# Kernel optimization log

Hardware: AMD Instinct MI355X
Metric: run time of the kernel (lower is better)

## Reference

```python
import jax, jax.numpy as jnp
import numpy as np

MAX_VAL = 255.0
C1 = (0.01 * MAX_VAL) ** 2
C2 = (0.03 * MAX_VAL) ** 2


def _gauss_window(ws, sigma, channel=3):
    x = np.arange(ws, dtype=np.float64)
    g = np.exp(-((x - ws // 2) ** 2) / (2.0 * sigma ** 2))
    g = g / g.sum()
    w2 = np.outer(g, g).astype(np.float32)  # [ws, ws]
    w = np.broadcast_to(w2, (channel, 1, ws, ws)).copy()  # depthwise OIHW
    return jnp.asarray(w)


def _dwconv(x, w, pad):
    # depthwise conv2d, NCHW, groups == channels
    return jax.lax.conv_general_dilated(
        x, w, window_strides=(1, 1), padding=[(pad, pad), (pad, pad)],
        dimension_numbers=("NCHW", "OIHW", "NCHW"),
        feature_group_count=x.shape[1])


def _ssim_pair(img1, img2):
    _, c, h, w = img1.shape
    ws = min(h, w, 11)
    sigma = 1.5 * ws / 11.0
    win = _gauss_window(ws, sigma, c)
    pad = ws // 2
    mu1 = _dwconv(img1, win, pad)
    mu2 = _dwconv(img2, win, pad)
    mu1_sq, mu2_sq, mu1_mu2 = mu1 * mu1, mu2 * mu2, mu1 * mu2
    sigma1_sq = _dwconv(img1 * img1, win, pad) - mu1_sq
    sigma2_sq = _dwconv(img2 * img2, win, pad) - mu2_sq
    sigma12 = _dwconv(img1 * img2, win, pad) - mu1_mu2
    V1 = 2.0 * sigma12 + C2
    V2 = sigma1_sq + sigma2_sq + C2
    ssim_map = (2.0 * mu1_mu2 + C1) * V1 / ((mu1_sq + mu2_sq + C1) * V2)
    mcs_map = V1 / V2
    return ssim_map.mean(), mcs_map.mean()


def _avg_pool2(x):
    B, C, H, W = x.shape
    return x.reshape(B, C, H // 2, 2, W // 2, 2).mean(axis=(3, 5))


def _ms_ssim(img1, img2, levels=5):
    weight = jnp.array([0.0448, 0.2856, 0.3001, 0.2363, 0.1333], jnp.float32)
    msssim, mcs = [], []
    for _ in range(levels):
        s, m = _ssim_pair(img1, img2)
        msssim.append(s)
        mcs.append(m)
        img1 = _avg_pool2(img1)
        img2 = _avg_pool2(img2)
    msssim = jnp.stack(msssim)
    mcs = jnp.stack(mcs)
    value = jnp.prod(mcs[: levels - 1] ** weight[: levels - 1]) * msssim[levels - 1] ** weight[levels - 1]
    return 1.0 - value


def _l1_oss(img1, img2):
    _, c, h, w = img1.shape
    ws = min(h, w, 7)
    sigma = 1.1 * ws / 7.0
    win = _gauss_window(ws, sigma, c)
    return _dwconv(jnp.abs(img1 - img2), win, ws // 2).mean()


def _clr_loss(img1, img3):
    _, c, h, w = img1.shape
    ws = min(h, w, 29)
    sigma = ws / 6.0
    win = _gauss_window(ws, sigma, c)
    pad = ws // 2
    mu1 = _dwconv(img1, win, pad)
    mu3 = _dwconv(img3, win, pad)
    cw = [-0.000519, 0.07633, -0.173433, 1.435936, -1.894404, 1.556091]
    # Horner evaluation of cw[5]*x^5 + ... + cw[1]*x + cw[0]
    mu1 = ((((cw[5] * mu1 + cw[4]) * mu1 + cw[3]) * mu1 + cw[2]) * mu1 + cw[1]) * mu1 + cw[0]
    wgray = jnp.array([0.299, 0.587, 0.144], jnp.float32).reshape(1, 3, 1, 1)
    mug1 = (mu1 * wgray).sum(axis=1, keepdims=True)  # 1x1 conv over channels
    mug3 = (mu3 * wgray).sum(axis=1, keepdims=True)
    me1 = mug1.mean(axis=(2, 3), keepdims=True)
    me3 = mug3.mean(axis=(2, 3), keepdims=True)
    sc = me1 / me3
    return jnp.abs(mu1 - mu3 * sc).mean()


def setup_inputs() -> dict:
    key = jax.random.key(0)
    k1, k2, k3 = jax.random.split(key, 3)
    shape = (16, 3, 512, 512)
    return {
        "img1": jax.random.uniform(k1, shape, dtype=jnp.float32),
        "img2": jax.random.uniform(k2, shape, dtype=jnp.float32),
        "img3": jax.random.uniform(k3, shape, dtype=jnp.float32),
    }


def reference(img1, img2, img3):
    l1v = _l1_oss(img1, img2)
    clrv = _clr_loss(img1, img3)
    ssimv = _ms_ssim(img1, img2)
    return 0.4 * ssimv + 0.4 * l1v + 0.2 * clrv
```

## Files before the change

### kernel.cpp

```cpp
#include <hip/hip_runtime.h>
#include <hip/hip_fp16.h>
#include <cmath>

typedef float f2 __attribute__((ext_vector_type(2)));

struct GW7  { float g[7];  };
struct GW11 { float g[11]; };
struct GW29 { float g[29]; };

static void make_gauss(int ws, double sigma, float* out) {
    double t[32]; double s = 0.0;
    int c = ws / 2;
    for (int i = 0; i < ws; ++i) { double d = i - c; t[i] = exp(-(d * d) / (2.0 * sigma * sigma)); s += t[i]; }
    for (int i = 0; i < ws; ++i) out[i] = (float)(t[i] / s);
}

#define ACC_SLOTS 44
#define ACC_BYTES (ACC_SLOTS * 64 * sizeof(double))

__device__ __forceinline__ float poly5(float x) {
    float r = fmaf(1.556091f, x, -1.894404f);
    r = fmaf(r, x, 1.435936f);
    r = fmaf(r, x, -0.173433f);
    r = fmaf(r, x, 0.07633f);
    r = fmaf(r, x, -0.000519f);
    return r;
}

__device__ __forceinline__ float border7(int p, const GW7& gw) {
    if (p >= 3 && p <= 508) return 1.f;
    float r = 0.f;
    #pragma unroll
    for (int k = 0; k < 7; ++k) { int q = p + 3 - k; if (q >= 0 && q < 512) r += gw.g[k]; }
    return r;
}

#define SSP 49
#define SRP 33
#define CLINE 33
#define CROWS 156

template<bool SRC2, bool INTERIOR>
__device__ __forceinline__ void ssim_tile(
    const float* __restrict__ Aim, const float* __restrict__ Bim,
    const f2* __restrict__ AB, int H, int plane, int ty, int tx,
    const GW11& gw, const GW7& g7, double* __restrict__ acc, int level,
    f2* __restrict__ pooled, int Ho, f2* lds, float* red, int bid)
{
    constexpr int IN = 42;
    f2* s    = lds;
    f2* r_mu = lds;
    f2* r_sq = lds + IN * SRP;

    const int tid = threadIdx.x;
    const size_t base = (size_t)plane * H * H;
    const int oy = ty * 32 - 5, ox = tx * 32 - 5;

    {
        int y = tid / 42;
        int x = tid - y * 42;
        #pragma unroll
        for (int it = 0; it < 7; ++it) {
            if (it < 6 || tid < 228) {
                f2 v;
                if (INTERIOR) {
                    size_t o = base + (size_t)(oy + y) * H + (ox + x);
                    if (SRC2) v = AB[o];
                    else { v.x = Aim[o]; v.y = Bim[o]; }
                } else {
                    int gy = oy + y, gx = ox + x;
                    bool ok = (gy >= 0) && (gy < H) && (gx >= 0) && (gx < H);
                    size_t o = base + (size_t)gy * H + gx;
                    v = (f2){0.f, 0.f};
                    if (ok) { if (SRC2) v = AB[o]; else { v.x = Aim[o]; v.y = Bim[o]; } }
                }
                s[y * SSP + x] = v;
            }
            y += 6; x += 4; if (x >= 42) { x -= 42; ++y; }
        }
    }
    __syncthreads();

    f2 v[18];
    const int ry = tid >> 2, rx0 = (tid & 3) * 8;
    if (tid < IN * 4) {
        #pragma unroll
        for (int l = 0; l < 18; ++l) v[l] = s[ry * SSP + rx0 + l];
    }
    if (pooled) {
        int py = tid >> 4, px = tid & 15;
        int a = (5 + 2 * py) * SSP + 5 + 2 * px;
        f2 u = s[a] + s[a + 1] + s[a + SSP] + s[a + SSP + 1];
        pooled[(size_t)plane * Ho * Ho + (size_t)(ty * 16 + py) * Ho + (tx * 16 + px)] = 0.25f * u;
    }
    float l1p = 0.f;
    if (level == 0) {
        #pragma unroll
        for (int jj = 0; jj < 4; ++jj) {
            int p = jj * 256 + tid;
            int py = p >> 5, px = p & 31;
            f2 u = s[(5 + py) * SSP + 5 + px];
            float d = fabsf(u.x - u.y);
            if (INTERIOR) l1p += d;
            else l1p += border7(ty * 32 + py, g7) * border7(tx * 32 + px, g7) * d;
        }
    }
    __syncthreads();

    if (tid < IN * 4) {
        #pragma unroll
        for (int j = 0; j < 8; ++j) {
            f2 a = {0.f, 0.f};
            #pragma unroll
            for (int k = 0; k < 11; ++k) a = gw.g[k] * v[j + k] + a;
            r_mu[ry * SRP + rx0 + j] = a;
        }
        #pragma unroll
        for (int l = 0; l < 18; ++l) {
            f2 w;
            w.x = fmaf(v[l].x, v[l].x, v[l].y * v[l].y);
            w.y = v[l].x * v[l].y;
            v[l] = w;
        }
        #pragma unroll
        for (int j = 0; j < 8; ++j) {
            f2 a = {0.f, 0.f};
            #pragma unroll
            for (int k = 0; k < 11; ++k) a = gw.g[k] * v[j + k] + a;
            r_sq[ry * SRP + rx0 + j] = a;
        }
    }
    __syncthreads();

    const int y0 = (tid >> 5) * 4, x = tid & 31;
    float lss = 0.f, lmc = 0.f;
    {
        f2 mu[4], q[4];
        {
            f2 u[14];
            #pragma unroll
            for (int l = 0; l < 14; ++l) u[l] = r_mu[(y0 + l) * SRP + x];
            #pragma unroll
            for (int j = 0; j < 4; ++j) {
                f2 a = {0.f, 0.f};
                #pragma unroll
                for (int k = 0; k < 11; ++k) a = gw.g[k] * u[j + k] + a;
                mu[j] = a;
            }
        }
        {
            f2 u[14];
            #pragma unroll
            for (int l = 0; l < 14; ++l) u[l] = r_sq[(y0 + l) * SRP + x];
            #pragma unroll
            for (int j = 0; j < 4; ++j) {
                f2 a = {0.f, 0.f};
                #pragma unroll
                for (int k = 0; k < 11; ++k) a = gw.g[k] * u[j + k] + a;
                q[j] = a;
            }
        }
        #pragma unroll
        for (int j = 0; j < 4; ++j) {
            float m1 = mu[j].x, m2 = mu[j].y;
            float P = m1 * m2;
            float S = fmaf(m1, m1, m2 * m2);
            float V1 = 2.f * (q[j].y - P) + 58.5225f;
            float V2 = (q[j].x - S) + 58.5225f;
            float num = (2.f * P + 6.5025f) * V1;
            float SC = S + 6.5025f;
            float inv = __builtin_amdgcn_rcpf(SC * V2);
            lss = fmaf(num, inv, lss);
            lmc = fmaf(V1 * SC, inv, lmc);
        }
    }
    #pragma unroll
    for (int o = 32; o > 0; o >>= 1) {
        lss += __shfl_down(lss, o); lmc += __shfl_down(lmc, o); l1p += __shfl_down(l1p, o);
    }
    if ((tid & 63) == 0) {
        int g = tid >> 6;
        red[g * 3] = lss; red[g * 3 + 1] = lmc; red[g * 3 + 2] = l1p;
    }
    __syncthreads();
    if (tid == 0) {
        float a = red[0] + red[3] + red[6] + red[9];
        float m = red[1] + red[4] + red[7] + red[10];
        int stripe = bid & 63;
        atomicAdd(&acc[(0 + level) * 64 + stripe], (double)a);
        atomicAdd(&acc[(5 + level) * 64 + stripe], (double)m);
        if (level == 0) {
            float l1 = red[2] + red[5] + red[8] + red[11];
            atomicAdd(&acc[10 * 64 + stripe], (double)l1);
        }
    }
}

template<bool SRC2>
__global__ __launch_bounds__(256, 8) void ssim_kernel(
    const float* __restrict__ Aim, const float* __restrict__ Bim, const f2* __restrict__ AB,
    int H, int tpp, int tilesX, GW11 gw, GW7 g7, double* __restrict__ acc, int level,
    f2* __restrict__ pooled, int Ho)
{
    __shared__ f2 lds[2 * 42 * SRP];
    __shared__ float red[12];
    const int bid = blockIdx.x;
    const int plane = bid / tpp;
    const int t = bid - plane * tpp;
    const int ty = t / tilesX, tx = t - ty * tilesX;
    const bool interior = (ty > 0) && (ty < tilesX - 1) && (tx > 0) && (tx < tilesX - 1);
    if (interior)
        ssim_tile<SRC2, true >(Aim, Bim, AB, H, plane, ty, tx, gw, g7, acc, level, pooled, Ho, lds, red, bid);
    else
        ssim_tile<SRC2, false>(Aim, Bim, AB, H, plane, ty, tx, gw, g7, acc, level, pooled, Ho, lds, red, bid);
}

template<bool CCLEAN>
__device__ __forceinline__ void clr_strip(
    const float* __restrict__ img1, const float* __restrict__ img3,
    int plane, int tx, int q, const GW29& gw, __half2* buf, float* red,
    double* __restrict__ acc, __half2* __restrict__ pbuf, int bid)
{
    const int tid = threadIdx.x;
    const int base_row = q * 128;
    const int b = plane / 3, c = plane - b * 3;
    const float wg = (c == 0) ? 0.299f : (c == 1 ? 0.587f : 0.144f);
    const size_t base = (size_t)plane * (512 * 512);
    const int rrow = tid >> 2, xq = tid & 3;
    const int c0 = tx * 8 + xq * 2 - 4;

    auto rowconv = [&](int rel) {
        __half2* dst = buf + (rel + 14) * CLINE + xq * 8;
        const int lr = base_row + rel;
        if (lr < 0 || lr >= 512) {
            #pragma unroll
            for (int j = 0; j < 8; ++j) dst[j] = __floats2half2_rn(0.f, 0.f);
            return;
        }
        const float4* row1 = (const float4*)(img1 + base + (size_t)lr * 512);
        const float4* row3 = (const float4*)(img3 + base + (size_t)lr * 512);
        float w[40];
        float o1[8];
        #pragma unroll
        for (int k = 0; k < 10; ++k) {
            float4 f;
            if (CCLEAN) f = row1[c0 + k];
            else {
                int cc = c0 + k;
                f = (float4){0.f, 0.f, 0.f, 0.f};
                if (cc >= 0 && cc < 128) f = row1[cc];
            }
            w[4 * k] = f.x; w[4 * k + 1] = f.y; w[4 * k + 2] = f.z; w[4 * k + 3] = f.w;
        }
        #pragma unroll
        for (int j = 0; j < 8; ++j) {
            float a = 0.f;
            #pragma unroll
            for (int k = 0; k < 29; ++k) a = fmaf(gw.g[k], w[2 + j + k], a);
            o1[j] = a;
        }
        #pragma unroll
        for (int k = 0; k < 10; ++k) {
            float4 f;
            if (CCLEAN) f = row3[c0 + k];
            else {
                int cc = c0 + k;
                f = (float4){0.f, 0.f, 0.f, 0.f};
                if (cc >= 0 && cc < 128) f = row3[cc];
            }
            w[4 * k] = f.x; w[4 * k + 1] = f.y; w[4 * k + 2] = f.z; w[4 * k + 3] = f.w;
        }
        #pragma unroll
        for (int j = 0; j < 8; ++j) {
            float a = 0.f;
            #pragma unroll
            for (int k = 0; k < 29; ++k) a = fmaf(gw.g[k], w[2 + j + k], a);
            dst[j] = __floats2half2_rn(o1[j], a);
        }
    };

    rowconv(-14 + rrow);
    __syncthreads();

    float p1 = 0.f, p3 = 0.f;
    const int x = tid & 31;
    #pragma unroll
    for (int ck = 0; ck < 2; ++ck) {
        int rel = 50 + 64 * ck + rrow;
        if (rel <= 141) rowconv(rel);
        __syncthreads();
        #pragma unroll
        for (int g = 0; g < 2; ++g) {
            const int y0 = 64 * ck + g * 32 + (tid >> 5) * 4;
            f2 u[32];
            #pragma unroll
            for (int l = 0; l < 32; ++l) {
                float2 tf = __half22float2(buf[(y0 + l) * CLINE + x]);
                u[l] = (f2){tf.x, tf.y};
            }
            #pragma unroll
            for (int j = 0; j < 4; ++j) {
                f2 a = {0.f, 0.f};
                #pragma unroll
                for (int k = 0; k < 29; ++k) a = gw.g[k] * u[j + k] + a;
                float p = poly5(a.x);
                p1 += p; p3 += a.y;
                pbuf[base + (size_t)(base_row + y0 + j) * 512 + (tx * 32 + x)] =
                    __floats2half2_rn(p, a.y);
            }
        }
    }

    p1 *= wg; p3 *= wg;
    #pragma unroll
    for (int o = 32; o > 0; o >>= 1) { p1 += __shfl_down(p1, o); p3 += __shfl_down(p3, o); }
    if ((tid & 63) == 0) { red[(tid >> 6) * 2] = p1; red[(tid >> 6) * 2 + 1] = p3; }
    __syncthreads();
    if (tid == 0) {
        float a1 = red[0] + red[2] + red[4] + red[6];
        float a3 = red[1] + red[3] + red[5] + red[7];
        int stripe = bid & 63;
        atomicAdd(&acc[(12 + b) * 64 + stripe], (double)a1);
        atomicAdd(&acc[(28 + b) * 64 + stripe], (double)a3);
    }
}

__global__ __launch_bounds__(256, 8) void fused_l0(
    const float* __restrict__ img1, const float* __restrict__ img2,
    const float* __restrict__ img3,
    GW11 g11, GW7 g7, GW29 g29,
    __half2* __restrict__ pbuf, f2* __restrict__ pooled, double* __restrict__ acc)
{
    __shared__ f2 lds[2 * 42 * SRP];
    __shared__ float red[12];
    const int bid = blockIdx.x;
    const int q5 = bid / 5;

    if (bid - q5 * 5 == 0) {
        const int cid = q5;
        __half2* buf = (__half2*)lds;
        const int plane = cid >> 6, rr = cid & 63;
        const int tx = rr >> 2, q = rr & 3;
        if (tx >= 1 && tx <= 14)
            clr_strip<true >(img1, img3, plane, tx, q, g29, buf, red, acc, pbuf, bid);
        else
            clr_strip<false>(img1, img3, plane, tx, q, g29, buf, red, acc, pbuf, bid);
        return;
    }

    const int sid = bid - q5 - 1;
    const int plane = sid >> 8;
    const int t = sid & 255;
    const int ty = t >> 4, tx = t & 15;
    const bool interior = (ty >= 1) && (ty <= 14) && (tx >= 1) && (tx <= 14);
    if (interior)
        ssim_tile<false, true >(img1, img2, nullptr, 512, plane, ty, tx, g11, g7, acc, 0, pooled, 256, lds, red, bid);
    else
        ssim_tile<false, false>(img1, img2, nullptr, 512, plane, ty, tx, g11, g7, acc, 0, pooled, 256, lds, red, bid);
}

#define CRP 33
#define RING 128
template<int MODE>
__global__ __launch_bounds__(256) void clr_conv(
    const float* __restrict__ img1, const float* __restrict__ img3,
    __half2* __restrict__ pbuf, GW29 gw, double* __restrict__ acc)
{
    __shared__ f2 r[RING * CRP];
    __shared__ float red[8];
    __shared__ float sc_sh;

    const int tid = threadIdx.x, bid = blockIdx.x;
    const int plane = bid >> 4, tx = bid & 15;
    const int b = plane / 3, c = plane - b * 3;
    const float wg = (c == 0) ? 0.299f : (c == 1 ? 0.587f : 0.144f);
    const size_t base = (size_t)plane * (512 * 512);

    if (MODE == 2 && tid < 64) {
        double m1 = acc[(12 + b) * 64 + tid];
        double m3 = acc[(28 + b) * 64 + tid];
        #pragma unroll
        for (int o = 32; o > 0; o >>= 1) { m1 += __shfl_down(m1, o); m3 += __shfl_down(m3, o); }
        if (tid == 0) sc_sh = (float)(m1 / m3);
    }

    const int rrow = tid >> 2, xq = tid & 3;
    const int c0 = tx * 8 + xq * 2 - 4;

    auto rowconv = [&](int lr) {
        const int ri = ((lr + RING) & (RING - 1)) * CRP + xq * 8;
        if (lr < 0 || lr >= 512) {
            #pragma unroll
            for (int j = 0; j < 8; ++j) r[ri + j] = (f2){0.f, 0.f};
            return;
        }
        const float4* row1 = (const float4*)(img1 + base + (size_t)lr * 512);
        const float4* row3 = (const float4*)(img3 + base + (size_t)lr * 512);
        float w[40];
        float o1[8];
        #pragma unroll
        for (int k = 0; k < 10; ++k) {
            int cc = c0 + k;
            float4 f = {0.f, 0.f, 0.f, 0.f};
            if (cc >= 0 && cc < 128) f = row1[cc];
            w[4 * k] = f.x; w[4 * k + 1] = f.y; w[4 * k + 2] = f.z; w[4 * k + 3] = f.w;
        }
        #pragma unroll
        for (int j = 0; j < 8; ++j) {
            float a = 0.f;
            #pragma unroll
            for (int k = 0; k < 29; ++k) a = fmaf(gw.g[k], w[2 + j + k], a);
            o1[j] = a;
        }
        #pragma unroll
        for (int k = 0; k < 10; ++k) {
            int cc = c0 + k;
            float4 f = {0.f, 0.f, 0.f, 0.f};
            if (cc >= 0 && cc < 128) f = row3[cc];
            w[4 * k] = f.x; w[4 * k + 1] = f.y; w[4 * k + 2] = f.z; w[4 * k + 3] = f.w;
        }
        #pragma unroll
        for (int j = 0; j < 8; ++j) {
            float a = 0.f;
            #pragma unroll
            for (int k = 0; k < 29; ++k) a = fmaf(gw.g[k], w[2 + j + k], a);
            r[ri + j] = (f2){o1[j], a};
        }
    };

    rowconv(-14 + rrow);
    __syncthreads();

    float p1 = 0.f, p3 = 0.f;
    const int x = tid & 31;
    #pragma unroll 1
    for (int ck = 0; ck < 8; ++ck) {
        {
            int lr = 50 + 64 * ck + rrow;
            if (lr <= 525) rowconv(lr);
        }
        __syncthreads();
        #pragma unroll
        for (int g = 0; g < 2; ++g) {
            const int y0 = 64 * ck + g * 32 + (tid >> 5) * 4;
            f2 u[32];
            #pragma unroll
            for (int l = 0; l < 32; ++l)
                u[l] = r[(((y0 - 14 + l) + RING) & (RING - 1)) * CRP + x];
            #pragma unroll
            for (int j = 0; j < 4; ++j) {
                f2 a = {0.f, 0.f};
                #pragma unroll
                for (int k = 0; k < 29; ++k) a = gw.g[k] * u[j + k] + a;
                float p = poly5(a.x);
                if (MODE == 2) {
                    p1 += fabsf(p - a.y * sc_sh);
                } else {
                    p1 += p; p3 += a.y;
                }
            }
        }
        if (ck < 7) __syncthreads();
    }

    if (MODE != 2) { p1 *= wg; p3 *= wg; }
    #pragma unroll
    for (int o = 32; o > 0; o >>= 1) { p1 += __shfl_down(p1, o); p3 += __shfl_down(p3, o); }
    if ((tid & 63) == 0) { red[(tid >> 6) * 2] = p1; red[(tid >> 6) * 2 + 1] = p3; }
    __syncthreads();
    if (tid == 0) {
        float a1 = red[0] + red[2] + red[4] + red[6];
        int stripe = bid & 63;
        if (MODE == 2) {
            atomicAdd(&acc[11 * 64 + stripe], (double)a1);
        } else {
            float a3 = red[1] + red[3] + red[5] + red[7];
            atomicAdd(&acc[(12 + b) * 64 + stripe], (double)a1);
            atomicAdd(&acc[(28 + b) * 64 + stripe], (double)a3);
        }
    }
}

__global__ __launch_bounds__(256) void clr_fin(
    const __half2* __restrict__ pbuf, double* __restrict__ acc)
{
    __shared__ float red[4];
    __shared__ float sc_sh;
    const int tid = threadIdx.x, bid = blockIdx.x;
    const int b = bid / 192, sub = bid - b * 192;
    if (tid < 64) {
        double m1 = acc[(12 + b) * 64 + tid];
        double m3 = acc[(28 + b) * 64 + tid];
        #pragma unroll
        for (int o = 32; o > 0; o >>= 1) { m1 += __shfl_down(m1, o); m3 += __shfl_down(m3, o); }
        if (tid == 0) sc_sh = (float)(m1 / m3);
    }
    __syncthreads();
    const float sc = sc_sh;
    const size_t bo = (size_t)b * 786432 + (size_t)sub * 4096;
    float s = 0.f;
    #pragma unroll
    for (int it = 0; it < 8; ++it) {
        size_t i = bo + it * 512 + tid * 2;
        float2 a = __half22float2(pbuf[i]);
        float2 c = __half22float2(pbuf[i + 1]);
        s += fabsf(a.x - a.y * sc) + fabsf(c.x - c.y * sc);
    }
    #pragma unroll
    for (int o = 32; o > 0; o >>= 1) s += __shfl_down(s, o);
    if ((tid & 63) == 0) red[tid >> 6] = s;
    __syncthreads();
    if (tid == 0)
        atomicAdd(&acc[11 * 64 + (bid & 63)], (double)(red[0] + red[1] + red[2] + red[3]));
}

__global__ void finalize_kernel(const double* __restrict__ acc, float* __restrict__ out)
{
    __shared__ double sums[ACC_SLOTS];
    int t = threadIdx.x;
    if (t < ACC_SLOTS) {
        double s = 0.0;
        for (int i = 0; i < 64; ++i) s += acc[t * 64 + i];
        sums[t] = s;
    }
    __syncthreads();
    if (t == 0) {
        const double w[5] = {0.0448, 0.2856, 0.3001, 0.2363, 0.1333};
        double value = 1.0;
        for (int l = 0; l < 5; ++l) {
            double dim = (double)(512 >> l);
            double cnt = 48.0 * dim * dim;
            double mval = (l < 4) ? (sums[5 + l] / cnt) : (sums[l] / cnt);
            value *= pow(mval, w[l]);
        }
        double n0 = 48.0 * 512.0 * 512.0;
        double l1v = sums[10] / n0;
        double clrv = sums[11] / n0;
        out[0] = (float)(0.4 * (1.0 - value) + 0.4 * l1v + 0.2 * clrv);
    }
}

extern "C" void kernel_launch(void* const* d_in, const int* in_sizes, int n_in,
                              void* d_out, int out_size, void* d_ws, size_t ws_size,
                              hipStream_t stream)
{
    (void)in_sizes; (void)n_in; (void)out_size;
    const float* img1 = (const float*)d_in[0];
    const float* img2 = (const float*)d_in[1];
    const float* img3 = (const float*)d_in[2];
    float* out = (float*)d_out;
    double* acc = (double*)d_ws;

    GW11 g11; make_gauss(11, 1.5, g11.g);
    GW7  g7;  make_gauss(7, 1.1, g7.g);
    GW29 g29; make_gauss(29, 29.0 / 6.0, g29.g);

    hipMemsetAsync(d_ws, 0, ACC_BYTES, stream);

    f2* pyr = (f2*)((char*)d_ws + 32768);
    size_t offs[4];
    offs[0] = 0;
    offs[1] = offs[0] + (size_t)48 * 256 * 256;
    offs[2] = offs[1] + (size_t)48 * 128 * 128;
    offs[3] = offs[2] + (size_t)48 * 64 * 64;
    const size_t PYRF2 = offs[3] + (size_t)48 * 32 * 32;

    const size_t poff = 32768 + PYRF2 * sizeof(f2);
    const size_t PBYTES = (size_t)48 * 512 * 512 * sizeof(__half2);
    __half2* pbuf = (__half2*)((char*)d_ws + poff);
    const bool bigws = (ws_size >= poff + PBYTES);

    if (bigws) {
        fused_l0<<<15360, 256, 0, stream>>>(img1, img2, img3, g11, g7, g29,
                                            pbuf, pyr + offs[0], acc);
    } else {
        ssim_kernel<false><<<12288, 256, 0, stream>>>(
            img1, img2, nullptr, 512, 256, 16, g11, g7, acc, 0, pyr + offs[0], 256);
        clr_conv<1><<<768, 256, 0, stream>>>(img1, img3, pbuf, g29, acc);
    }

    const f2* cur = pyr + offs[0];
    int H = 256;
    for (int l = 1; l < 5; ++l) {
        int tilesX = H / 32; int tpp = tilesX * tilesX;
        f2* pooled = (l < 4) ? (pyr + offs[l]) : nullptr;
        int Ho = H / 2;
        ssim_kernel<true><<<48 * tpp, 256, 0, stream>>>(
            nullptr, nullptr, cur, H, tpp, tilesX, g11, g7, acc, l, pooled, Ho);
        cur = pooled; H = Ho;
    }

    if (bigws) {
        clr_fin<<<3072, 256, 0, stream>>>(pbuf, acc);
    } else {
        clr_conv<2><<<768, 256, 0, stream>>>(img1, img3, pbuf, g29, acc);
    }

    finalize_kernel<<<1, 64, 0, stream>>>(acc, out);
}
```

Measured before the change: 217.4 us.

## Drop interior/border template specializations, streaming vertical conv, relax launch bounds

```diff
diff --git a/kernel.cpp b/kernel.cpp
--- a/kernel.cpp
+++ b/kernel.cpp
@@ -40,7 +40,7 @@
 #define CLINE 33
 #define CROWS 156
 
-template<bool SRC2, bool INTERIOR>
+template<bool SRC2>
 __device__ __forceinline__ void ssim_tile(
     const float* __restrict__ Aim, const float* __restrict__ Bim,
     const f2* __restrict__ AB, int H, int plane, int ty, int tx,
@@ -56,28 +56,17 @@
     const size_t base = (size_t)plane * H * H;
     const int oy = ty * 32 - 5, ox = tx * 32 - 5;
 
-    {
-        int y = tid / 42;
-        int x = tid - y * 42;
-        #pragma unroll
-        for (int it = 0; it < 7; ++it) {
-            if (it < 6 || tid < 228) {
-                f2 v;
-                if (INTERIOR) {
-                    size_t o = base + (size_t)(oy + y) * H + (ox + x);
-                    if (SRC2) v = AB[o];
-                    else { v.x = Aim[o]; v.y = Bim[o]; }
-                } else {
-                    int gy = oy + y, gx = ox + x;
-                    bool ok = (gy >= 0) && (gy < H) && (gx >= 0) && (gx < H);
-                    size_t o = base + (size_t)gy * H + gx;
-                    v = (f2){0.f, 0.f};
-                    if (ok) { if (SRC2) v = AB[o]; else { v.x = Aim[o]; v.y = Bim[o]; } }
-                }
-                s[y * SSP + x] = v;
-            }
-            y += 6; x += 4; if (x >= 42) { x -= 42; ++y; }
-        }
+    for (int i = tid; i < IN * IN; i += 256) {
+        int y = i / IN, x = i - y * IN;
+        int gy = oy + y, gx = ox + x;
+        bool ok = (gy >= 0) && (gy < H) && (gx >= 0) && (gx < H);
+        size_t o = base + (size_t)gy * H + gx;
+        f2 v = {0.f, 0.f};
+        if (ok) {
+            if (SRC2) v = AB[o];
+            else { v.x = Aim[o]; v.y = Bim[o]; }
+        }
+        s[y * SSP + x] = v;
     }
     __syncthreads();
 
@@ -100,9 +89,7 @@
             int p = jj * 256 + tid;
             int py = p >> 5, px = p & 31;
             f2 u = s[(5 + py) * SSP + 5 + px];
-            float d = fabsf(u.x - u.y);
-            if (INTERIOR) l1p += d;
-            else l1p += border7(ty * 32 + py, g7) * border7(tx * 32 + px, g7) * d;
+            l1p += border7(ty * 32 + py, g7) * border7(tx * 32 + px, g7) * fabsf(u.x - u.y);
         }
     }
     __syncthreads();
@@ -197,7 +184,7 @@
 }
 
 template<bool SRC2>
-__global__ __launch_bounds__(256, 8) void ssim_kernel(
+__global__ __launch_bounds__(256) void ssim_kernel(
     const float* __restrict__ Aim, const float* __restrict__ Bim, const f2* __restrict__ AB,
     int H, int tpp, int tilesX, GW11 gw, GW7 g7, double* __restrict__ acc, int level,
     f2* __restrict__ pooled, int Ho)
@@ -208,14 +195,9 @@
     const int plane = bid / tpp;
     const int t = bid - plane * tpp;
     const int ty = t / tilesX, tx = t - ty * tilesX;
-    const bool interior = (ty > 0) && (ty < tilesX - 1) && (tx > 0) && (tx < tilesX - 1);
-    if (interior)
-        ssim_tile<SRC2, true >(Aim, Bim, AB, H, plane, ty, tx, gw, g7, acc, level, pooled, Ho, lds, red, bid);
-    else
-        ssim_tile<SRC2, false>(Aim, Bim, AB, H, plane, ty, tx, gw, g7, acc, level, pooled, Ho, lds, red, bid);
-}
-
-template<bool CCLEAN>
+    ssim_tile<SRC2>(Aim, Bim, AB, H, plane, ty, tx, gw, g7, acc, level, pooled, Ho, lds, red, bid);
+}
+
 __device__ __forceinline__ void clr_strip(
     const float* __restrict__ img1, const float* __restrict__ img3,
     int plane, int tx, int q, const GW29& gw, __half2* buf, float* red,
@@ -243,13 +225,9 @@
         float o1[8];
         #pragma unroll
         for (int k = 0; k < 10; ++k) {
-            float4 f;
-            if (CCLEAN) f = row1[c0 + k];
-            else {
-                int cc = c0 + k;
-                f = (float4){0.f, 0.f, 0.f, 0.f};
-                if (cc >= 0 && cc < 128) f = row1[cc];
-            }
+            int cc = c0 + k;
+            float4 f = {0.f, 0.f, 0.f, 0.f};
+            if (cc >= 0 && cc < 128) f = row1[cc];
             w[4 * k] = f.x; w[4 * k + 1] = f.y; w[4 * k + 2] = f.z; w[4 * k + 3] = f.w;
         }
         #pragma unroll
@@ -261,13 +239,9 @@
         }
         #pragma unroll
         for (int k = 0; k < 10; ++k) {
-            float4 f;
-            if (CCLEAN) f = row3[c0 + k];
-            else {
-                int cc = c0 + k;
-                f = (float4){0.f, 0.f, 0.f, 0.f};
-                if (cc >= 0 && cc < 128) f = row3[cc];
-            }
+            int cc = c0 + k;
+            float4 f = {0.f, 0.f, 0.f, 0.f};
+            if (cc >= 0 && cc < 128) f = row3[cc];
             w[4 * k] = f.x; w[4 * k + 1] = f.y; w[4 * k + 2] = f.z; w[4 * k + 3] = f.w;
         }
         #pragma unroll
@@ -292,21 +266,23 @@
         #pragma unroll
         for (int g = 0; g < 2; ++g) {
             const int y0 = 64 * ck + g * 32 + (tid >> 5) * 4;
-            f2 u[32];
+            f2 mu[4];
+            #pragma unroll
+            for (int j = 0; j < 4; ++j) mu[j] = (f2){0.f, 0.f};
             #pragma unroll
             for (int l = 0; l < 32; ++l) {
                 float2 tf = __half22float2(buf[(y0 + l) * CLINE + x]);
-                u[l] = (f2){tf.x, tf.y};
+                f2 val = {tf.x, tf.y};
+                #pragma unroll
+                for (int j = 0; j < 4; ++j)
+                    if (l - j >= 0 && l - j < 29) mu[j] = gw.g[l - j] * val + mu[j];
             }
             #pragma unroll
             for (int j = 0; j < 4; ++j) {
-                f2 a = {0.f, 0.f};
-                #pragma unroll
-                for (int k = 0; k < 29; ++k) a = gw.g[k] * u[j + k] + a;
-                float p = poly5(a.x);
-                p1 += p; p3 += a.y;
+                float p = poly5(mu[j].x);
+                p1 += p; p3 += mu[j].y;
                 pbuf[base + (size_t)(base_row + y0 + j) * 512 + (tx * 32 + x)] =
-                    __floats2half2_rn(p, a.y);
+                    __floats2half2_rn(p, mu[j].y);
             }
         }
     }
@@ -325,7 +301,7 @@
     }
 }
 
-__global__ __launch_bounds__(256, 8) void fused_l0(
+__global__ __launch_bounds__(256) void fused_l0(
     const float* __restrict__ img1, const float* __restrict__ img2,
     const float* __restrict__ img3,
     GW11 g11, GW7 g7, GW29 g29,
@@ -341,10 +317,7 @@
         __half2* buf = (__half2*)lds;
         const int plane = cid >> 6, rr = cid & 63;
         const int tx = rr >> 2, q = rr & 3;
-        if (tx >= 1 && tx <= 14)
-            clr_strip<true >(img1, img3, plane, tx, q, g29, buf, red, acc, pbuf, bid);
-        else
-            clr_strip<false>(img1, img3, plane, tx, q, g29, buf, red, acc, pbuf, bid);
+        clr_strip(img1, img3, plane, tx, q, g29, buf, red, acc, pbuf, bid);
         return;
     }
 
@@ -352,11 +325,7 @@
     const int plane = sid >> 8;
     const int t = sid & 255;
     const int ty = t >> 4, tx = t & 15;
-    const bool interior = (ty >= 1) && (ty <= 14) && (tx >= 1) && (tx <= 14);
-    if (interior)
-        ssim_tile<false, true >(img1, img2, nullptr, 512, plane, ty, tx, g11, g7, acc, 0, pooled, 256, lds, red, bid);
-    else
-        ssim_tile<false, false>(img1, img2, nullptr, 512, plane, ty, tx, g11, g7, acc, 0, pooled, 256, lds, red, bid);
+    ssim_tile<false>(img1, img2, nullptr, 512, plane, ty, tx, g11, g7, acc, 0, pooled, 256, lds, red, bid);
 }
 
 #define CRP 33
@@ -443,20 +412,23 @@
         #pragma unroll
         for (int g = 0; g < 2; ++g) {
             const int y0 = 64 * ck + g * 32 + (tid >> 5) * 4;
-            f2 u[32];
-            #pragma unroll
-            for (int l = 0; l < 32; ++l)
-                u[l] = r[(((y0 - 14 + l) + RING) & (RING - 1)) * CRP + x];
+            f2 mu[4];
+            #pragma unroll
+            for (int j = 0; j < 4; ++j) mu[j] = (f2){0.f, 0.f};
+            #pragma unroll
+            for (int l = 0; l < 32; ++l) {
+                f2 val = r[(((y0 - 14 + l) + RING) & (RING - 1)) * CRP + x];
+                #pragma unroll
+                for (int j = 0; j < 4; ++j)
+                    if (l - j >= 0 && l - j < 29) mu[j] = gw.g[l - j] * val + mu[j];
+            }
             #pragma unroll
             for (int j = 0; j < 4; ++j) {
-                f2 a = {0.f, 0.f};
-                #pragma unroll
-                for (int k = 0; k < 29; ++k) a = gw.g[k] * u[j + k] + a;
-                float p = poly5(a.x);
+                float p = poly5(mu[j].x);
                 if (MODE == 2) {
-                    p1 += fabsf(p - a.y * sc_sh);
+                    p1 += fabsf(p - mu[j].y * sc_sh);
                 } else {
-                    p1 += p; p3 += a.y;
+                    p1 += p; p3 += mu[j].y;
                 }
             }
         }
```

After: 223.3 us. +2.7%, slower.
